# Performance work log

Hardware: AMD Instinct MI355X
Metric: run time of the kernel (lower is better)

## Reference

```python
import jax, jax.numpy as jnp
import numpy as np

B, NCLASS, ATTN, CH = 256, 1000, 32, 512
P = 0.5  # exchange probability threshold


def setup_inputs() -> dict:
    key = jax.random.key(0)
    k1, k2, k3, k4 = jax.random.split(key, 4)
    features = jax.random.normal(k1, (B, ATTN, CH), dtype=jnp.float32)
    idx = jax.random.randint(k2, (B,), 0, NCLASS)
    labels = jax.nn.one_hot(idx, NCLASS, dtype=jnp.float32)  # one-hot class labels
    anchor = jax.random.normal(k3, (NCLASS, ATTN, CH), dtype=jnp.float32)
    cache = jnp.zeros((NCLASS, ATTN, CH), dtype=jnp.float32)
    count = jnp.zeros((NCLASS,), dtype=jnp.float32)
    rand_u = jax.random.uniform(k4, (B, ATTN), dtype=jnp.float32)  # replaces torch.rand in forward
    return {"features": features, "labels": labels, "anchor": anchor,
            "cache": cache, "count": count, "rand_u": rand_u}


def reference(features, labels, anchor, cache, count, rand_u):
    # label-weighted outer-product accumulate: (B,A,C) x (B,N) -> (N,A,C)
    # (torch materializes (B,N,A,C) via broadcast; this is the fused contraction)
    batch_cache = jnp.einsum('bac,bn->nac', features, labels)
    new_cache = cache + batch_cache
    new_count = count + labels.sum(axis=0)
    # exchange: random per-(sample, attention-part) blend with class anchor
    mask = (rand_u > P).astype(features.dtype)[:, :, None]  # (B,A,1)
    cls = jnp.argmax(labels, axis=1)                         # (B,)
    exch_features = mask * anchor[cls] + (1.0 - mask) * features
    return exch_features, new_cache, new_count
```

## Files before the change

kernel.cpp:

```cpp
#include <hip/hip_runtime.h>

typedef float f32x4 __attribute__((ext_vector_type(4)));

constexpr int kB  = 256;
constexpr int kN  = 1000;
constexpr int kA  = 32;
constexpr int kC  = 512;
constexpr int kAC = kA * kC;
constexpr int kFeat  = kB * kAC;
constexpr int kCache = kN * kAC;
constexpr int kRows  = kB * kA;

constexpr int kCacheSplit = 4;
constexpr int kCacheBlks  = kN * kCacheSplit;
constexpr int kF4PerClass = kAC / 4;
constexpr int kF4PerChunk = kF4PerClass / kCacheSplit;
constexpr int kAccN       = kF4PerChunk / 256;

constexpr int kExRowsPerBlk = 8;
constexpr int kExBlks = kRows / kExRowsPerBlk;
constexpr int kExIters = kExRowsPerBlk * 128 / 256;

__global__ __launch_bounds__(256) void k_prep(
    const float* __restrict__ labels,
    const float* __restrict__ rand_u,
    int* __restrict__ cls,
    int* __restrict__ srcrow)
{
    const int wave = threadIdx.x >> 6;
    const int lane = threadIdx.x & 63;
    const int b = blockIdx.x * 4 + wave;
    const float* row = labels + (size_t)b * kN;
    float best = -3.4e38f;
    int   bidx = kN;
    for (int n = lane; n < kN; n += 64) {
        float v = row[n];
        if (v > best) { best = v; bidx = n; }
    }
    #pragma unroll
    for (int off = 32; off >= 1; off >>= 1) {
        float ov = __shfl_xor(best, off, 64);
        int   oi = __shfl_xor(bidx, off, 64);
        if (ov > best || (ov == best && oi < bidx)) { best = ov; bidx = oi; }
    }
    if (lane == 0) cls[b] = bidx;
    if (lane < kA) {
        const int r = b * kA + lane;
        const float ru = rand_u[r];
        srcrow[r] = (ru > 0.5f) ? (int)(0x80000000u | (unsigned)(bidx * kA + lane))
                                : r;
    }
}

__global__ __launch_bounds__(256) void k_cache(
    const float* __restrict__ features,
    const float* __restrict__ cache,
    const float* __restrict__ count,
    const int*   __restrict__ cls,
    float* __restrict__ out_cache,
    float* __restrict__ out_count)
{
    const int blk = blockIdx.x;
    const int t = threadIdx.x;
    const int n = blk >> 2;
    const int q = blk & 3;

    __shared__ unsigned long long masks[4];
    const int myc = cls[t];
    unsigned long long mb = __ballot(myc == n);
    if ((t & 63) == 0) masks[t >> 6] = mb;
    __syncthreads();

    unsigned long long m[4];
    int mtot = 0;
    #pragma unroll
    for (int w = 0; w < 4; ++w) { m[w] = masks[w]; mtot += __popcll(m[w]); }

    const size_t base = (size_t)n * kF4PerClass + (size_t)q * kF4PerChunk;
    const f32x4* src = (const f32x4*)cache + base;
    f32x4*       dst = (f32x4*)out_cache + base;

    f32x4 v0 = src[t];
    f32x4 v1 = src[t + 256];
    f32x4 v2 = src[t + 512];
    f32x4 v3 = src[t + 768];

    #pragma unroll
    for (int w = 0; w < 4; ++w) {
        unsigned long long mm = m[w];
        while (mm) {
            const int bit = __ffsll((long long)mm) - 1;
            mm &= mm - 1;
            const int b = w * 64 + bit;
            const f32x4* f = (const f32x4*)features
                            + (size_t)b * kF4PerClass + (size_t)q * kF4PerChunk;
            f32x4 f0 = f[t];
            f32x4 f1 = f[t + 256];
            f32x4 f2 = f[t + 512];
            f32x4 f3 = f[t + 768];
            v0 += f0; v1 += f1; v2 += f2; v3 += f3;
        }
    }

    __builtin_nontemporal_store(v0, &dst[t]);
    __builtin_nontemporal_store(v1, &dst[t + 256]);
    __builtin_nontemporal_store(v2, &dst[t + 512]);
    __builtin_nontemporal_store(v3, &dst[t + 768]);

    if (t == 0 && q == 0) out_count[n] = count[n] + (float)mtot;
}

__global__ __launch_bounds__(256) void k_exch(
    const float* __restrict__ features,
    const float* __restrict__ anchor,
    const int*   __restrict__ srcrow,
    float* __restrict__ out_feat)
{
    const int t  = threadIdx.x;
    const int j0 = blockIdx.x * (kExRowsPerBlk * 128);
    const f32x4* features4 = (const f32x4*)features;
    const f32x4* anchor4   = (const f32x4*)anchor;
    f32x4*       out4      = (f32x4*)out_feat;

    int s[kExIters];
    #pragma unroll
    for (int k = 0; k < kExIters; ++k)
        s[k] = srcrow[(j0 + k * 256 + t) >> 7];

    f32x4 v[kExIters];
    #pragma unroll
    for (int k = 0; k < kExIters; ++k) {
        const int c4 = (j0 + k * 256 + t) & 127;
        const f32x4* srcb = (s[k] >= 0) ? features4 : anchor4;
        v[k] = srcb[(size_t)(s[k] & 0x7fffffff) * 128 + c4];
    }
    #pragma unroll
    for (int k = 0; k < kExIters; ++k)
        __builtin_nontemporal_store(v[k], &out4[j0 + k * 256 + t]);
}

extern "C" void kernel_launch(void* const* d_in, const int* in_sizes, int n_in,
                              void* d_out, int out_size, void* d_ws, size_t ws_size,
                              hipStream_t stream) {
    const float* features = (const float*)d_in[0];
    const float* labels   = (const float*)d_in[1];
    const float* anchor   = (const float*)d_in[2];
    const float* cache    = (const float*)d_in[3];
    const float* count    = (const float*)d_in[4];
    const float* rand_u   = (const float*)d_in[5];

    float* out_feat  = (float*)d_out;
    float* out_cache = out_feat + kFeat;
    float* out_count = out_cache + kCache;

    int* cls    = (int*)d_ws;
    int* srcrow = cls + kB;

    k_prep<<<kB / 4, 256, 0, stream>>>(labels, rand_u, cls, srcrow);
    k_cache<<<kCacheBlks, 256, 0, stream>>>(features, cache, count, cls,
                                            out_cache, out_count);
    k_exch<<<kExBlks, 256, 0, stream>>>(features, anchor, srcrow, out_feat);
}
```

Baseline: 203.4 us.

## Fuse cache accumulate and exchange into one tiled kernel with precomputed class masks

Adds a small planning kernel that builds per-class sample bitmasks and counts once, replacing the ballot over all 256 labels that every cache block used to repeat. The cache-accumulate and exchange-gather kernels are merged into a single launch over a combined tile space, with each tile twice as large (8 vec4 loads per thread). Nontemporal stores become regular stores. This removes one launch and lets the two bandwidth-bound phases overlap, at the cost of an extra tiny kernel and larger tiles with fewer blocks.

```diff
diff --git a/kernel.cpp b/kernel.cpp
--- a/kernel.cpp
+++ b/kernel.cpp
@@ -11,15 +11,16 @@
 constexpr int kCache = kN * kAC;
 constexpr int kRows  = kB * kA;
 
-constexpr int kCacheSplit = 4;
-constexpr int kCacheBlks  = kN * kCacheSplit;
 constexpr int kF4PerClass = kAC / 4;
-constexpr int kF4PerChunk = kF4PerClass / kCacheSplit;
-constexpr int kAccN       = kF4PerChunk / 256;
+constexpr int kTileF4 = 2048;
+constexpr int kATiles = (kCache / 4) / kTileF4;
+constexpr int kBTiles = (kFeat  / 4) / kTileF4;
+constexpr int kTiles  = kATiles + kBTiles;
 
-constexpr int kExRowsPerBlk = 8;
-constexpr int kExBlks = kRows / kExRowsPerBlk;
-constexpr int kExIters = kExRowsPerBlk * 128 / 256;
+constexpr int kWsMasksOff  = 0;
+constexpr int kWsClsOff    = 32000;
+constexpr int kWsSrcrowOff = 33024;
+constexpr int kWsCntOff    = 65792;
 
 __global__ __launch_bounds__(256) void k_prep(
     const float* __restrict__ labels,
@@ -52,91 +53,116 @@
     }
 }
 
-__global__ __launch_bounds__(256) void k_cache(
-    const float* __restrict__ features,
-    const float* __restrict__ cache,
+__global__ __launch_bounds__(256) void k_plan(
+    const int*   __restrict__ cls,
     const float* __restrict__ count,
-    const int*   __restrict__ cls,
-    float* __restrict__ out_cache,
+    unsigned long long* __restrict__ masks,
+    int*   __restrict__ cnt,
     float* __restrict__ out_count)
 {
-    const int blk = blockIdx.x;
-    const int t = threadIdx.x;
-    const int n = blk >> 2;
-    const int q = blk & 3;
-
-    __shared__ unsigned long long masks[4];
-    const int myc = cls[t];
-    unsigned long long mb = __ballot(myc == n);
-    if ((t & 63) == 0) masks[t >> 6] = mb;
+    __shared__ int scls[kB];
+    scls[threadIdx.x] = cls[threadIdx.x];
     __syncthreads();
 
-    unsigned long long m[4];
-    int mtot = 0;
+    const int n = blockIdx.x * 256 + threadIdx.x;
+    if (n >= kN) return;
+
+    unsigned long long m[4] = {0, 0, 0, 0};
     #pragma unroll
-    for (int w = 0; w < 4; ++w) { m[w] = masks[w]; mtot += __popcll(m[w]); }
+    for (int w = 0; w < 4; ++w)
+        for (int b = 0; b < 64; ++b)
+            m[w] |= (unsigned long long)(scls[w * 64 + b] == n) << b;
 
-    const size_t base = (size_t)n * kF4PerClass + (size_t)q * kF4PerChunk;
-    const f32x4* src = (const f32x4*)cache + base;
-    f32x4*       dst = (f32x4*)out_cache + base;
-
-    f32x4 v0 = src[t];
-    f32x4 v1 = src[t + 256];
-    f32x4 v2 = src[t + 512];
-    f32x4 v3 = src[t + 768];
-
+    int tot = 0;
     #pragma unroll
-    for (int w = 0; w < 4; ++w) {
-        unsigned long long mm = m[w];
-        while (mm) {
-            const int bit = __ffsll((long long)mm) - 1;
-            mm &= mm - 1;
-            const int b = w * 64 + bit;
-            const f32x4* f = (const f32x4*)features
-                            + (size_t)b * kF4PerClass + (size_t)q * kF4PerChunk;
-            f32x4 f0 = f[t];
-            f32x4 f1 = f[t + 256];
-            f32x4 f2 = f[t + 512];
-            f32x4 f3 = f[t + 768];
-            v0 += f0; v1 += f1; v2 += f2; v3 += f3;
-        }
-    }
-
-    __builtin_nontemporal_store(v0, &dst[t]);
-    __builtin_nontemporal_store(v1, &dst[t + 256]);
-    __builtin_nontemporal_store(v2, &dst[t + 512]);
-    __builtin_nontemporal_store(v3, &dst[t + 768]);
-
-    if (t == 0 && q == 0) out_count[n] = count[n] + (float)mtot;
+    for (int w = 0; w < 4; ++w) { masks[n * 4 + w] = m[w]; tot += __popcll(m[w]); }
+    cnt[n] = tot;
+    out_count[n] = count[n] + (float)tot;
 }
 
-__global__ __launch_bounds__(256) void k_exch(
+__global__ __launch_bounds__(256) void k_main(
     const float* __restrict__ features,
     const float* __restrict__ anchor,
+    const float* __restrict__ cache,
     const int*   __restrict__ srcrow,
-    float* __restrict__ out_feat)
+    const unsigned long long* __restrict__ masks,
+    const int*   __restrict__ cnt,
+    float* __restrict__ out_feat,
+    float* __restrict__ out_cache)
 {
-    const int t  = threadIdx.x;
-    const int j0 = blockIdx.x * (kExRowsPerBlk * 128);
-    const f32x4* features4 = (const f32x4*)features;
-    const f32x4* anchor4   = (const f32x4*)anchor;
-    f32x4*       out4      = (f32x4*)out_feat;
+    const int t    = threadIdx.x;
+    const int tile = blockIdx.x;
+    if (tile < kATiles) {
+        const int n    = tile >> 1;
+        const int half = tile & 1;
+        const size_t base = (size_t)n * kF4PerClass + (size_t)half * kTileF4;
+        const f32x4* src = (const f32x4*)cache + base;
+        f32x4*       dst = (f32x4*)out_cache + base;
 
-    int s[kExIters];
-    #pragma unroll
-    for (int k = 0; k < kExIters; ++k)
-        s[k] = srcrow[(j0 + k * 256 + t) >> 7];
+        const int c = cnt[n];
+        f32x4 v0 = src[t];
+        f32x4 v1 = src[t + 256];
+        f32x4 v2 = src[t + 512];
+        f32x4 v3 = src[t + 768];
+        f32x4 v4 = src[t + 1024];
+        f32x4 v5 = src[t + 1280];
+        f32x4 v6 = src[t + 1536];
+        f32x4 v7 = src[t + 1792];
 
-    f32x4 v[kExIters];
-    #pragma unroll
-    for (int k = 0; k < kExIters; ++k) {
-        const int c4 = (j0 + k * 256 + t) & 127;
-        const f32x4* srcb = (s[k] >= 0) ? features4 : anchor4;
-        v[k] = srcb[(size_t)(s[k] & 0x7fffffff) * 128 + c4];
+        if (c) {
+            #pragma unroll
+            for (int w = 0; w < 4; ++w) {
+                unsigned long long mm = masks[n * 4 + w];
+                while (mm) {
+                    const int bit = __ffsll((long long)mm) - 1;
+                    mm &= mm - 1;
+                    const int b = w * 64 + bit;
+                    const f32x4* f = (const f32x4*)features
+                                    + (size_t)b * kF4PerClass + (size_t)half * kTileF4;
+                    f32x4 f0 = f[t];
+                    f32x4 f1 = f[t + 256];
+                    f32x4 f2 = f[t + 512];
+                    f32x4 f3 = f[t + 768];
+                    f32x4 f4 = f[t + 1024];
+                    f32x4 f5 = f[t + 1280];
+                    f32x4 f6 = f[t + 1536];
+                    f32x4 f7 = f[t + 1792];
+                    v0 += f0; v1 += f1; v2 += f2; v3 += f3;
+                    v4 += f4; v5 += f5; v6 += f6; v7 += f7;
+                }
+            }
+        }
+        dst[t]        = v0;
+        dst[t + 256]  = v1;
+        dst[t + 512]  = v2;
+        dst[t + 768]  = v3;
+        dst[t + 1024] = v4;
+        dst[t + 1280] = v5;
+        dst[t + 1536] = v6;
+        dst[t + 1792] = v7;
+    } else {
+        const int bt = tile - kATiles;
+        const int u0 = bt * kTileF4 + t;
+        const f32x4* features4 = (const f32x4*)features;
+        const f32x4* anchor4   = (const f32x4*)anchor;
+        f32x4*       out4      = (f32x4*)out_feat;
+
+        int s[8];
+        #pragma unroll
+        for (int i = 0; i < 8; ++i)
+            s[i] = srcrow[(u0 + i * 256) >> 7];
+
+        f32x4 v[8];
+        #pragma unroll
+        for (int i = 0; i < 8; ++i) {
+            const int c4 = (u0 + i * 256) & 127;
+            const f32x4* sb = (s[i] >= 0) ? features4 : anchor4;
+            v[i] = sb[(size_t)(s[i] & 0x7fffffff) * 128 + c4];
+        }
+        #pragma unroll
+        for (int i = 0; i < 8; ++i)
+            out4[u0 + i * 256] = v[i];
     }
-    #pragma unroll
-    for (int k = 0; k < kExIters; ++k)
-        __builtin_nontemporal_store(v[k], &out4[j0 + k * 256 + t]);
 }
 
 extern "C" void kernel_launch(void* const* d_in, const int* in_sizes, int n_in,
@@ -153,11 +179,14 @@
     float* out_cache = out_feat + kFeat;
     float* out_count = out_cache + kCache;
 
-    int* cls    = (int*)d_ws;
-    int* srcrow = cls + kB;
+    char* ws = (char*)d_ws;
+    unsigned long long* masks = (unsigned long long*)(ws + kWsMasksOff);
+    int* cls    = (int*)(ws + kWsClsOff);
+    int* srcrow = (int*)(ws + kWsSrcrowOff);
+    int* cnt    = (int*)(ws + kWsCntOff);
 
     k_prep<<<kB / 4, 256, 0, stream>>>(labels, rand_u, cls, srcrow);
-    k_cache<<<kCacheBlks, 256, 0, stream>>>(features, cache, count, cls,
-                                            out_cache, out_count);
-    k_exch<<<kExBlks, 256, 0, stream>>>(features, anchor, srcrow, out_feat);
+    k_plan<<<4, 256, 0, stream>>>(cls, count, masks, cnt, out_count);
+    k_main<<<kTiles, 256, 0, stream>>>(features, anchor, cache, srcrow,
+                                       masks, cnt, out_feat, out_cache);
 }
```

New measurement: 206.3 us. About the same (+1.4%).
